# Optimization experiments

Hardware: AMD Instinct MI355X
Metric: run time of the kernel (lower is better)

## Reference

```python
import jax, jax.numpy as jnp
import numpy as np

D_MODEL = 1024
N_HEADS = 16
D_KV = 64
N_CONTEXT = 20
PASSAGE_LEN = 200
BSZ = 8
QLEN = 32
KLEN = N_CONTEXT * PASSAGE_LEN


def setup_inputs() -> dict:
    key = jax.random.key(0)
    ks = jax.random.split(key, 8)
    inp = {
        "input": jax.random.normal(ks[0], (BSZ, QLEN, D_MODEL), jnp.float32),
        "kv": jax.random.normal(ks[1], (BSZ, KLEN, D_MODEL), jnp.float32),
        "mask_add": jnp.zeros((BSZ, 1, 1, KLEN), jnp.float32),
        "mask_bool": jnp.ones((BSZ, 1, 1, KLEN), bool),
        "position_bias": jax.random.normal(ks[2], (1, N_HEADS, QLEN, KLEN), jnp.float32),
        "Wq": jax.random.normal(ks[3], (D_MODEL, N_HEADS * D_KV), jnp.float32) * 0.02,
        "Wk": jax.random.normal(ks[4], (D_MODEL, N_HEADS * D_KV), jnp.float32) * 0.02,
        "Wv": jax.random.normal(ks[5], (D_MODEL, N_HEADS * D_KV), jnp.float32) * 0.02,
        "Wo": jax.random.normal(ks[6], (N_HEADS * D_KV, D_MODEL), jnp.float32) * 0.02,
        "n_context": N_CONTEXT,
    }
    return inp


def reference(input, kv, mask_add, mask_bool, position_bias, Wq, Wk, Wv, Wo, n_context):
    b, qlen, dm = input.shape
    klen = kv.shape[1]
    H = position_bias.shape[1]
    dh = Wq.shape[1] // H
    # projections, [b, h, len, dh]
    q = (input @ Wq).reshape(b, qlen, H, dh).transpose(0, 2, 1, 3)
    k = (kv @ Wk).reshape(b, klen, H, dh).transpose(0, 2, 1, 3)
    v = (kv @ Wv).reshape(b, klen, H, dh).transpose(0, 2, 1, 3)
    # unscaled T5-style attention scores + additive mask + position bias
    scores = jnp.einsum('bhqd,bhkd->bhqk', q, k) + mask_add + position_bias
    attn = jax.nn.softmax(scores.astype(jnp.float32), axis=-1).astype(scores.dtype)
    # dropout p=0 (eval) -> identity
    out = jnp.einsum('bhqk,bhkd->bhqd', attn, v)
    out = out.transpose(0, 2, 1, 3).reshape(b, qlen, H * dh) @ Wo
    # collect_cross_attention(sum_over_tokens=True): masked avg of raw scores per context
    s = scores.reshape(b, H, qlen, n_context, -1)
    m = mask_bool.reshape(b, 1, 1, n_context, -1).astype(scores.dtype)
    collected = (s * m).sum(-1) / m.sum(-1)  # [b, H, qlen, n_context]
    return out, collected
```

## Files before the change

### kernel.cpp

```cpp
#include <hip/hip_runtime.h>
#include <stdint.h>

constexpr int DMODEL = 1024;
constexpr int NH     = 16;
constexpr int DHD    = 64;
constexpr int BS     = 8;
constexpr int QLEN   = 32;
constexpr int KLEN   = 4000;
constexpr int NCTX   = 20;
constexpr int PLEN   = 200;

typedef __bf16 bf16_t;
typedef bf16_t bf16x8 __attribute__((ext_vector_type(8)));
typedef float  f32x4  __attribute__((ext_vector_type(4)));

__device__ __forceinline__ uint16_t f2bf(float f) {
  uint32_t u = __float_as_uint(f);
  u += 0x7FFF + ((u >> 16) & 1);
  return (uint16_t)(u >> 16);
}

#define GLOAD_LDS16(gsrc, ldst) \
  __builtin_amdgcn_global_load_lds((const __attribute__((address_space(1))) void*)(gsrc), \
                                   (__attribute__((address_space(3))) void*)(ldst), 16, 0, 0)

__global__ void detect_mask(const uint32_t* __restrict__ m, int* __restrict__ flag) {
  if (threadIdx.x == 0 && blockIdx.x == 0)
    *flag = (m[0] == 0x01010101u) ? 1 : 0;
}

__global__ void cast_inputs(const float* __restrict__ kv, const float* __restrict__ inp,
                            uint16_t* __restrict__ kv16, uint16_t* __restrict__ in16) {
  const int NKV4 = (BS * KLEN * DMODEL) / 4;
  const int NIN4 = (BS * QLEN * DMODEL) / 4;
  const int total = NKV4 + NIN4;
  for (int i = blockIdx.x * blockDim.x + threadIdx.x; i < total; i += gridDim.x * blockDim.x) {
    float4 v; uint16_t* dst; int di;
    if (i < NKV4) { v = ((const float4*)kv)[i]; dst = kv16; di = i; }
    else          { v = ((const float4*)inp)[i - NKV4]; dst = in16; di = i - NKV4; }
    ushort4 o; o.x = f2bf(v.x); o.y = f2bf(v.y); o.z = f2bf(v.z); o.w = f2bf(v.w);
    ((ushort4*)dst)[di] = o;
  }
}

__global__ void wtrans(const float* __restrict__ w0, const float* __restrict__ w1,
                       const float* __restrict__ w2, const float* __restrict__ w3,
                       uint16_t* __restrict__ out) {
  __shared__ uint16_t sm[64][65];
  const float* W = (blockIdx.z == 0) ? w0 : (blockIdx.z == 1) ? w1 : (blockIdx.z == 2) ? w2 : w3;
  uint16_t* o = out + (size_t)blockIdx.z * DMODEL * DMODEL;
  int k0 = blockIdx.y * 64, n0 = blockIdx.x * 64;
  int t = threadIdx.x;
  for (int i = 0; i < 16; ++i) {
    int s = t + i * 256; int r = s >> 6, c = s & 63;
    sm[r][c] = f2bf(W[(size_t)(k0 + r) * DMODEL + n0 + c]);
  }
  __syncthreads();
  for (int i = 0; i < 16; ++i) {
    int s = t + i * 256; int r = s >> 6, c = s & 63;
    o[(size_t)(n0 + r) * DMODEL + k0 + c] = sm[c][r];
  }
}

template <int OUT_F32>
__global__ void __launch_bounds__(256) gemm_bt(const uint16_t* __restrict__ A,
                                               const uint16_t* __restrict__ Bt,
                                               void* __restrict__ Cv,
                                               int M, int N, int K) {
  __shared__ __align__(16) uint16_t As[128 * 32];
  __shared__ __align__(16) uint16_t Bs[128 * 32];
  const int m0 = blockIdx.x * 128, n0 = blockIdx.y * 128;
  const int tid = threadIdx.x, lane = tid & 63, wave = tid >> 6;
  const int wm = wave >> 1, wn = wave & 1;
  const int l15 = lane & 15, g = lane >> 4;
  const int sr = lane >> 2, sc = (lane & 3) * 8;
  const int c0 = wave * 2, c1 = wave * 2 + 1;
  f32x4 acc[4][4] = {};
  const int KT = K / 32;
  for (int kt = 0; kt < KT; ++kt) {
    __syncthreads();
    GLOAD_LDS16(A  + (size_t)(m0 + c0 * 16 + sr) * K + kt * 32 + sc, As + c0 * 512);
    GLOAD_LDS16(A  + (size_t)(m0 + c1 * 16 + sr) * K + kt * 32 + sc, As + c1 * 512);
    GLOAD_LDS16(Bt + (size_t)(n0 + c0 * 16 + sr) * K + kt * 32 + sc, Bs + c0 * 512);
    GLOAD_LDS16(Bt + (size_t)(n0 + c1 * 16 + sr) * K + kt * 32 + sc, Bs + c1 * 512);
    __syncthreads();
    bf16x8 a[4], b[4];
#pragma unroll
    for (int i = 0; i < 4; ++i)
      a[i] = *(const bf16x8*)&As[(wm * 64 + i * 16 + l15) * 32 + g * 8];
#pragma unroll
    for (int j = 0; j < 4; ++j)
      b[j] = *(const bf16x8*)&Bs[(wn * 64 + j * 16 + l15) * 32 + g * 8];
#pragma unroll
    for (int i = 0; i < 4; ++i)
#pragma unroll
      for (int j = 0; j < 4; ++j)
        acc[i][j] = __builtin_amdgcn_mfma_f32_16x16x32_bf16(a[i], b[j], acc[i][j], 0, 0, 0);
  }
#pragma unroll
  for (int i = 0; i < 4; ++i)
#pragma unroll
    for (int j = 0; j < 4; ++j) {
      int row = m0 + wm * 64 + i * 16 + g * 4;
      int col = n0 + wn * 64 + j * 16 + l15;
      if (OUT_F32) {
        float* C = (float*)Cv;
#pragma unroll
        for (int r = 0; r < 4; ++r) C[(size_t)(row + r) * N + col] = acc[i][j][r];
      } else {
        uint16_t* C = (uint16_t*)Cv;
#pragma unroll
        for (int r = 0; r < 4; ++r) C[(size_t)(row + r) * N + col] = f2bf(acc[i][j][r]);
      }
    }
}

__global__ void __launch_bounds__(512) gemm_kv(const uint16_t* __restrict__ A,
                                               const uint16_t* __restrict__ Bt,
                                               uint16_t* __restrict__ kmat,
                                               uint16_t* __restrict__ vt) {
  __shared__ __align__(16) uint16_t smem[65536];
  const int orig = blockIdx.x;
  const int swz  = (orig & 7) * 125 + (orig >> 3);
  const int mb = swz >> 3, nb = swz & 7;
  const int m0 = mb * 256, n0 = nb * 256;
  const int tid = threadIdx.x, lane = tid & 63, wid = tid >> 6;
  const int wm = wid >> 2, wn = wid & 3;
  const int l15 = lane & 15, g = lane >> 4;
  const int l3 = lane >> 3, l7 = lane & 7;
  const int cg = (l7 ^ (l3 & 7)) * 8;

  f32x4 acc[8][4] = {};

#define ABASE(bf) (smem + (bf) * 32768)
#define BBASE(bf) (smem + (bf) * 32768 + 16384)

  auto STAGE = [&](int bf, int kt) {
    const int colg = kt * 64 + cg;
#pragma unroll
    for (int ia = 0; ia < 4; ++ia) {
      const int r0 = wid * 32 + ia * 8;
      GLOAD_LDS16(A + (size_t)(m0 + r0 + l3) * 1024 + colg, ABASE(bf) + r0 * 64);
    }
#pragma unroll
    for (int ib = 0; ib < 4; ++ib) {
      const int r0 = wid * 32 + ib * 8;
      GLOAD_LDS16(Bt + (size_t)(n0 + r0 + l3) * 1024 + colg, BBASE(bf) + r0 * 64);
    }
  };

  STAGE(0, 0);
  for (int kt = 0; kt < 16; ++kt) {
    const int bf = kt & 1;
    if (kt < 15) {
      STAGE(bf ^ 1, kt + 1);
      asm volatile("s_waitcnt vmcnt(8)" ::: "memory");
    } else {
      asm volatile("s_waitcnt vmcnt(0)" ::: "memory");
    }
    asm volatile("s_barrier" ::: "memory");
#pragma unroll
    for (int kk = 0; kk < 2; ++kk) {
      bf16x8 af[8], bb[4];
#pragma unroll
      for (int mi = 0; mi < 8; ++mi) {
        const int row = wm * 128 + mi * 16 + l15;
        const int gr = (kk * 4 + g) ^ (row & 7);
        af[mi] = *(const bf16x8*)&ABASE(bf)[row * 64 + gr * 8];
      }
#pragma unroll
      for (int ni = 0; ni < 4; ++ni) {
        const int row = wn * 64 + ni * 16 + l15;
        const int gr = (kk * 4 + g) ^ (row & 7);
        bb[ni] = *(const bf16x8*)&BBASE(bf)[row * 64 + gr * 8];
      }
#pragma unroll
      for (int mi = 0; mi < 8; ++mi)
#pragma unroll
        for (int ni = 0; ni < 4; ++ni)
          acc[mi][ni] = __builtin_amdgcn_mfma_f32_16x16x32_bf16(af[mi], bb[ni], acc[mi][ni], 0, 0, 0);
    }
    asm volatile("s_barrier" ::: "memory");
  }
#undef ABASE
#undef BBASE

  if (n0 < 1024) {
#pragma unroll
    for (int mi = 0; mi < 8; ++mi)
#pragma unroll
      for (int ni = 0; ni < 4; ++ni) {
        const int row = m0 + wm * 128 + mi * 16 + g * 4;
        const int col = n0 + wn * 64 + ni * 16 + l15;
#pragma unroll
        for (int r = 0; r < 4; ++r)
          kmat[(size_t)(row + r) * 1024 + col] = f2bf(acc[mi][ni][r]);
      }
  } else {
#pragma unroll
    for (int mi = 0; mi < 8; ++mi)
#pragma unroll
      for (int ni = 0; ni < 4; ++ni) {
        const int dd = wn * 64 + ni * 16 + l15;
        const int kk_tok = wm * 128 + mi * 16 + g * 4;
#pragma unroll
        for (int r = 0; r < 4; ++r)
          smem[dd * 256 + kk_tok + r] = f2bf(acc[mi][ni][r]);
      }
    __syncthreads();
    const int hbase = (n0 - 1024) >> 6;
#pragma unroll
    for (int it = 0; it < 16; ++it) {
      const int sp = it * 512 + tid;
      const int dd = sp >> 5, kk0 = (sp & 31) * 8;
      const int grow = m0 + kk0;
      const int b = grow / 4000, krel = grow - b * 4000;
      const int h = hbase + (dd >> 6), d = dd & 63;
      ulonglong2 v = *(const ulonglong2*)&smem[dd * 256 + kk0];
      *(ulonglong2*)&vt[(((size_t)(b * NH + h) * DHD + d) * KLEN) + krel] = v;
    }
  }
}

__global__ void __launch_bounds__(256) fused_attn(const uint16_t* __restrict__ Q,
                                                  const uint16_t* __restrict__ Km,
                                                  const uint16_t* __restrict__ Vt,
                                                  const float* __restrict__ mask_add,
                                                  const void* __restrict__ maskb,
                                                  const int* __restrict__ flag,
                                                  const float* __restrict__ bias,
                                                  float* __restrict__ part,
                                                  float* __restrict__ coll) {
  __shared__ __align__(16) uint16_t plds[4][32 * 32];
  const int kc = blockIdx.x, h = blockIdx.y, b = blockIdx.z;
  const int lane = threadIdx.x & 63, wave = threadIdx.x >> 6;
  const int l15 = lane & 15, g = lane >> 4;
  const int ctx = kc * 4 + wave;
  const int kbase = ctx * PLEN;
  const int fm = *flag;

  bf16x8 aq[2][2];
#pragma unroll
  for (int i = 0; i < 2; ++i)
#pragma unroll
    for (int ks = 0; ks < 2; ++ks)
      aq[i][ks] = *(const bf16x8*)&Q[(size_t)(b * QLEN + i * 16 + l15) * DMODEL + h * DHD + ks * 32 + g * 8];

  f32x4 o[2][4] = {};
  float mr[2][4], lr[2][4], cs[2][4];
#pragma unroll
  for (int i = 0; i < 2; ++i)
#pragma unroll
    for (int r = 0; r < 4; ++r) { mr[i][r] = -3e38f; lr[i][r] = 0.f; cs[i][r] = 0.f; }
  float cnt = 0.f;

  for (int t = 0; t < 7; ++t) {
    const int k0 = kbase + t * 32;
    bf16x8 kb[2][2];
#pragma unroll
    for (int j = 0; j < 2; ++j) {
      int kr = k0 + j * 16 + l15; if (kr > KLEN - 1) kr = KLEN - 1;
#pragma unroll
      for (int ks = 0; ks < 2; ++ks)
        kb[j][ks] = *(const bf16x8*)&Km[(size_t)(b * KLEN + kr) * DMODEL + h * DHD + ks * 32 + g * 8];
    }
    f32x4 sa[2][2] = {};
#pragma unroll
    for (int ks = 0; ks < 2; ++ks)
#pragma unroll
      for (int i = 0; i < 2; ++i)
#pragma unroll
        for (int j = 0; j < 2; ++j)
          sa[i][j] = __builtin_amdgcn_mfma_f32_16x16x32_bf16(aq[i][ks], kb[j][ks], sa[i][j], 0, 0, 0);

    int colc[2]; bool vd[2], vm[2]; float ma[2];
#pragma unroll
    for (int j = 0; j < 2; ++j) {
      int col = k0 + j * 16 + l15;
      vd[j] = (col < kbase + PLEN);
      int cc = col; if (cc > KLEN - 1) cc = KLEN - 1;
      colc[j] = cc;
      ma[j] = mask_add[b * KLEN + cc];
      bool mk = fm ? (((const uint8_t*)maskb)[b * KLEN + cc] != 0)
                   : (((const int*)maskb)[b * KLEN + cc] != 0);
      vm[j] = vd[j] && mk;
    }

    float sv[2][2][4];
    float tmax[2][4];
#pragma unroll
    for (int i = 0; i < 2; ++i)
#pragma unroll
      for (int r = 0; r < 4; ++r) {
        tmax[i][r] = -3e38f;
        const int q = i * 16 + g * 4 + r;
        const size_t brow = (size_t)(h * QLEN + q) * KLEN;
#pragma unroll
        for (int j = 0; j < 2; ++j) {
          float raw = sa[i][j][r] + ma[j] + bias[brow + colc[j]];
          cs[i][r] += vm[j] ? raw : 0.f;
          float x = vd[j] ? raw : -3e38f;
          sv[i][j][r] = x;
          tmax[i][r] = fmaxf(tmax[i][r], x);
        }
      }
#pragma unroll
    for (int j = 0; j < 2; ++j) cnt += vm[j] ? 1.f : 0.f;

#pragma unroll
    for (int i = 0; i < 2; ++i)
#pragma unroll
      for (int r = 0; r < 4; ++r) {
        float v = tmax[i][r];
        v = fmaxf(v, __shfl_xor(v, 1)); v = fmaxf(v, __shfl_xor(v, 2));
        v = fmaxf(v, __shfl_xor(v, 4)); v = fmaxf(v, __shfl_xor(v, 8));
        tmax[i][r] = v;
      }
    float scale[2][4];
#pragma unroll
    for (int i = 0; i < 2; ++i)
#pragma unroll
      for (int r = 0; r < 4; ++r) {
        float mn = fmaxf(mr[i][r], tmax[i][r]);
        scale[i][r] = __expf(mr[i][r] - mn);
        mr[i][r] = mn;
        lr[i][r] *= scale[i][r];
      }
#pragma unroll
    for (int i = 0; i < 2; ++i)
#pragma unroll
      for (int j2 = 0; j2 < 4; ++j2)
#pragma unroll
        for (int r = 0; r < 4; ++r)
          o[i][j2][r] *= scale[i][r];
#pragma unroll
    for (int i = 0; i < 2; ++i)
#pragma unroll
      for (int r = 0; r < 4; ++r) {
        const int q = i * 16 + g * 4 + r;
#pragma unroll
        for (int j = 0; j < 2; ++j) {
          float p = __expf(sv[i][j][r] - mr[i][r]);
          lr[i][r] += p;
          plds[wave][q * 32 + j * 16 + l15] = f2bf(p);
        }
      }
    bf16x8 ap[2];
#pragma unroll
    for (int i = 0; i < 2; ++i)
      ap[i] = *(const bf16x8*)&plds[wave][(i * 16 + l15) * 32 + g * 8];
    bf16x8 vb[4];
    int vc = k0 + g * 8; if (vc > KLEN - 8) vc = KLEN - 8;
#pragma unroll
    for (int j2 = 0; j2 < 4; ++j2)
      vb[j2] = *(const bf16x8*)&Vt[((size_t)((b * NH + h) * DHD + j2 * 16 + l15)) * KLEN + vc];
#pragma unroll
    for (int i = 0; i < 2; ++i)
#pragma unroll
      for (int j2 = 0; j2 < 4; ++j2)
        o[i][j2] = __builtin_amdgcn_mfma_f32_16x16x32_bf16(ap[i], vb[j2], o[i][j2], 0, 0, 0);
  }

#pragma unroll
  for (int i = 0; i < 2; ++i)
#pragma unroll
    for (int r = 0; r < 4; ++r) {
      float v = lr[i][r];
      v += __shfl_xor(v, 1); v += __shfl_xor(v, 2); v += __shfl_xor(v, 4); v += __shfl_xor(v, 8);
      lr[i][r] = v;
      float c = cs[i][r];
      c += __shfl_xor(c, 1); c += __shfl_xor(c, 2); c += __shfl_xor(c, 4); c += __shfl_xor(c, 8);
      cs[i][r] = c;
    }
  { float c = cnt; c += __shfl_xor(c, 1); c += __shfl_xor(c, 2); c += __shfl_xor(c, 4); c += __shfl_xor(c, 8); cnt = c; }

  float* pr = part + ((size_t)((b * NH + h) * NCTX + ctx)) * 32 * 72;
#pragma unroll
  for (int i = 0; i < 2; ++i)
#pragma unroll
    for (int j2 = 0; j2 < 4; ++j2)
#pragma unroll
      for (int r = 0; r < 4; ++r)
        pr[(i * 16 + g * 4 + r) * 72 + 8 + j2 * 16 + l15] = o[i][j2][r];
  if (l15 == 0) {
#pragma unroll
    for (int i = 0; i < 2; ++i)
#pragma unroll
      for (int r = 0; r < 4; ++r) {
        int q = i * 16 + g * 4 + r;
        pr[q * 72 + 0] = mr[i][r];
        pr[q * 72 + 1] = lr[i][r];
        coll[(((size_t)(b * NH + h)) * QLEN + q) * NCTX + ctx] = cs[i][r] / cnt;
      }
  }
}

__global__ void __launch_bounds__(256) combine_attn(const float* __restrict__ part,
                                                    uint16_t* __restrict__ ao16) {
  const int t = threadIdx.x;
  const int row = blockIdx.x * 16 + (t >> 4);
  const int ln = t & 15;
  const int bh = row >> 5, q = row & 31;
  const float* p0 = part + ((size_t)bh * 640 + q) * 72;
  float M = -3e38f;
#pragma unroll
  for (int c = 0; c < NCTX; ++c) M = fmaxf(M, p0[(size_t)c * 2304]);
  float Z = 0.f, o0 = 0.f, o1 = 0.f, o2 = 0.f, o3 = 0.f;
  const int d0 = ln * 4;
  for (int c = 0; c < NCTX; ++c) {
    const float* pc = p0 + (size_t)c * 2304;
    float e = __expf(pc[0] - M);
    Z += e * pc[1];
    float4 ov = *(const float4*)&pc[8 + d0];
    o0 += e * ov.x; o1 += e * ov.y; o2 += e * ov.z; o3 += e * ov.w;
  }
  float iz = 1.f / Z;
  const int b = bh >> 4, h = bh & 15;
  ushort4 w; w.x = f2bf(o0 * iz); w.y = f2bf(o1 * iz); w.z = f2bf(o2 * iz); w.w = f2bf(o3 * iz);
  *(ushort4*)&ao16[(size_t)(b * QLEN + q) * DMODEL + h * DHD + d0] = w;
}

extern "C" void kernel_launch(void* const* d_in, const int* in_sizes, int n_in,
                              void* d_out, int out_size, void* d_ws, size_t ws_size,
                              hipStream_t stream) {
  const float* input     = (const float*)d_in[0];
  const float* kv        = (const float*)d_in[1];
  const float* mask_add  = (const float*)d_in[2];
  const void*  mask_bool = d_in[3];
  const float* bias      = (const float*)d_in[4];
  const float* Wq        = (const float*)d_in[5];
  const float* Wk        = (const float*)d_in[6];
  const float* Wv        = (const float*)d_in[7];
  const float* Wo        = (const float*)d_in[8];
  float* out  = (float*)d_out;
  float* coll = out + (size_t)BS * QLEN * DMODEL;

  char* ws = (char*)d_ws;
  size_t off = 0;
  auto alloc = [&](size_t bytes) { char* p = ws + off; off += (bytes + 255) & ~(size_t)255; return p; };
  uint16_t* kv16 = (uint16_t*)alloc((size_t)BS * KLEN * DMODEL * 2);
  uint16_t* in16 = (uint16_t*)alloc((size_t)BS * QLEN * DMODEL * 2);
  uint16_t* wt   = (uint16_t*)alloc((size_t)4 * DMODEL * DMODEL * 2);
  uint16_t* q16  = (uint16_t*)alloc((size_t)BS * QLEN * DMODEL * 2);
  uint16_t* kmat = (uint16_t*)alloc((size_t)BS * KLEN * DMODEL * 2);
  uint16_t* vt   = (uint16_t*)alloc((size_t)BS * KLEN * DMODEL * 2);
  float*    part = (float*)   alloc((size_t)BS * NH * NCTX * 32 * 72 * 4);
  uint16_t* ao16 = (uint16_t*)alloc((size_t)BS * QLEN * DMODEL * 2);
  int*      flag = (int*)alloc(256);

  uint16_t* WqT  = wt;
  uint16_t* WkvT = wt + (size_t)DMODEL * DMODEL;
  uint16_t* WoT  = wt + (size_t)3 * DMODEL * DMODEL;

  detect_mask<<<1, 64, 0, stream>>>((const uint32_t*)mask_bool, flag);
  cast_inputs<<<2048, 256, 0, stream>>>(kv, input, kv16, in16);
  wtrans<<<dim3(16, 16, 4), 256, 0, stream>>>(Wq, Wk, Wv, Wo, wt);
  gemm_bt<0><<<dim3(2, 8), 256, 0, stream>>>(in16, WqT, q16, BS * QLEN, DMODEL, DMODEL);
  gemm_kv<<<1000, 512, 0, stream>>>(kv16, WkvT, kmat, vt);
  fused_attn<<<dim3(5, NH, BS), 256, 0, stream>>>(q16, kmat, vt, mask_add, mask_bool, flag,
                                                  bias, part, coll);
  combine_attn<<<256, 256, 0, stream>>>(part, ao16);
  gemm_bt<1><<<dim3(2, 8), 256, 0, stream>>>(ao16, WoT, out, BS * QLEN, DMODEL, DMODEL);
}
```

Baseline: 305.3 us.

## Fuse fp32-to-bf16 cast of kv into the K/V projection GEMM loader

Removes the separate cast pass over the large kv tensor. The K/V GEMM now reads fp32 kv directly, converts it to bf16 with packed conversion instructions, and writes it into swizzled LDS. This avoids writing and re-reading a bf16 copy of kv. In exchange, the A-operand load is no longer an async global-to-LDS prefetch: it is a synchronous register load in the same iteration, so it loses the overlap with compute and doubles A read bytes per tile. Each kv row is also re-read and re-converted by every N-block.

```diff
diff --git a/kernel.cpp b/kernel.cpp
--- a/kernel.cpp
+++ b/kernel.cpp
@@ -29,18 +29,11 @@
     *flag = (m[0] == 0x01010101u) ? 1 : 0;
 }
 
-__global__ void cast_inputs(const float* __restrict__ kv, const float* __restrict__ inp,
-                            uint16_t* __restrict__ kv16, uint16_t* __restrict__ in16) {
-  const int NKV4 = (BS * KLEN * DMODEL) / 4;
-  const int NIN4 = (BS * QLEN * DMODEL) / 4;
-  const int total = NKV4 + NIN4;
-  for (int i = blockIdx.x * blockDim.x + threadIdx.x; i < total; i += gridDim.x * blockDim.x) {
-    float4 v; uint16_t* dst; int di;
-    if (i < NKV4) { v = ((const float4*)kv)[i]; dst = kv16; di = i; }
-    else          { v = ((const float4*)inp)[i - NKV4]; dst = in16; di = i - NKV4; }
-    ushort4 o; o.x = f2bf(v.x); o.y = f2bf(v.y); o.z = f2bf(v.z); o.w = f2bf(v.w);
-    ((ushort4*)dst)[di] = o;
-  }
+__global__ void cast_in16(const float* __restrict__ inp, uint16_t* __restrict__ in16) {
+  int i = blockIdx.x * blockDim.x + threadIdx.x;
+  float4 v = ((const float4*)inp)[i];
+  ushort4 o; o.x = f2bf(v.x); o.y = f2bf(v.y); o.z = f2bf(v.z); o.w = f2bf(v.w);
+  ((ushort4*)in16)[i] = o;
 }
 
 __global__ void wtrans(const float* __restrict__ w0, const float* __restrict__ w1,
@@ -115,7 +108,7 @@
     }
 }
 
-__global__ void __launch_bounds__(512) gemm_kv(const uint16_t* __restrict__ A,
+__global__ void __launch_bounds__(512) gemm_kv(const float* __restrict__ A,
                                                const uint16_t* __restrict__ Bt,
                                                uint16_t* __restrict__ kmat,
                                                uint16_t* __restrict__ vt) {
@@ -130,33 +123,47 @@
   const int l3 = lane >> 3, l7 = lane & 7;
   const int cg = (l7 ^ (l3 & 7)) * 8;
 
+  int ar0 = tid >> 3;
   f32x4 acc[8][4] = {};
 
 #define ABASE(bf) (smem + (bf) * 32768)
 #define BBASE(bf) (smem + (bf) * 32768 + 16384)
 
-  auto STAGE = [&](int bf, int kt) {
-    const int colg = kt * 64 + cg;
-#pragma unroll
-    for (int ia = 0; ia < 4; ++ia) {
-      const int r0 = wid * 32 + ia * 8;
-      GLOAD_LDS16(A + (size_t)(m0 + r0 + l3) * 1024 + colg, ABASE(bf) + r0 * 64);
-    }
+  auto STAGE_B = [&](int bf, int kt) {
 #pragma unroll
     for (int ib = 0; ib < 4; ++ib) {
       const int r0 = wid * 32 + ib * 8;
-      GLOAD_LDS16(Bt + (size_t)(n0 + r0 + l3) * 1024 + colg, BBASE(bf) + r0 * 64);
+      GLOAD_LDS16(Bt + (size_t)(n0 + r0 + l3) * 1024 + kt * 64 + cg, BBASE(bf) + r0 * 64);
     }
   };
 
-  STAGE(0, 0);
+  STAGE_B(0, 0);
   for (int kt = 0; kt < 16; ++kt) {
     const int bf = kt & 1;
+    float4 a8[8];
+#pragma unroll
+    for (int p = 0; p < 4; ++p) {
+      const int s = p * 512 + tid, r = s >> 3, gw = s & 7;
+      const float* src = A + (size_t)(m0 + r) * 1024 + kt * 64 + gw * 8;
+      a8[2 * p]     = *(const float4*)(src);
+      a8[2 * p + 1] = *(const float4*)(src + 4);
+    }
+#pragma unroll
+    for (int p = 0; p < 4; ++p) {
+      const int s = p * 512 + tid, r = s >> 3, gw = s & 7;
+      uint32_t w0, w1, w2, w3;
+      asm("v_cvt_pk_bf16_f32 %0, %1, %2" : "=v"(w0) : "v"(a8[2 * p].x),     "v"(a8[2 * p].y));
+      asm("v_cvt_pk_bf16_f32 %0, %1, %2" : "=v"(w1) : "v"(a8[2 * p].z),     "v"(a8[2 * p].w));
+      asm("v_cvt_pk_bf16_f32 %0, %1, %2" : "=v"(w2) : "v"(a8[2 * p + 1].x), "v"(a8[2 * p + 1].y));
+      asm("v_cvt_pk_bf16_f32 %0, %1, %2" : "=v"(w3) : "v"(a8[2 * p + 1].z), "v"(a8[2 * p + 1].w));
+      uint4 wv; wv.x = w0; wv.y = w1; wv.z = w2; wv.w = w3;
+      *(uint4*)&ABASE(bf)[r * 64 + (gw ^ (r & 7)) * 8] = wv;
+    }
     if (kt < 15) {
-      STAGE(bf ^ 1, kt + 1);
-      asm volatile("s_waitcnt vmcnt(8)" ::: "memory");
+      STAGE_B(bf ^ 1, kt + 1);
+      asm volatile("s_waitcnt vmcnt(4) lgkmcnt(0)" ::: "memory");
     } else {
-      asm volatile("s_waitcnt vmcnt(0)" ::: "memory");
+      asm volatile("s_waitcnt vmcnt(0) lgkmcnt(0)" ::: "memory");
     }
     asm volatile("s_barrier" ::: "memory");
 #pragma unroll
@@ -438,7 +445,6 @@
   char* ws = (char*)d_ws;
   size_t off = 0;
   auto alloc = [&](size_t bytes) { char* p = ws + off; off += (bytes + 255) & ~(size_t)255; return p; };
-  uint16_t* kv16 = (uint16_t*)alloc((size_t)BS * KLEN * DMODEL * 2);
   uint16_t* in16 = (uint16_t*)alloc((size_t)BS * QLEN * DMODEL * 2);
   uint16_t* wt   = (uint16_t*)alloc((size_t)4 * DMODEL * DMODEL * 2);
   uint16_t* q16  = (uint16_t*)alloc((size_t)BS * QLEN * DMODEL * 2);
@@ -453,10 +459,10 @@
   uint16_t* WoT  = wt + (size_t)3 * DMODEL * DMODEL;
 
   detect_mask<<<1, 64, 0, stream>>>((const uint32_t*)mask_bool, flag);
-  cast_inputs<<<2048, 256, 0, stream>>>(kv, input, kv16, in16);
+  cast_in16<<<256, 256, 0, stream>>>(input, in16);
   wtrans<<<dim3(16, 16, 4), 256, 0, stream>>>(Wq, Wk, Wv, Wo, wt);
   gemm_bt<0><<<dim3(2, 8), 256, 0, stream>>>(in16, WqT, q16, BS * QLEN, DMODEL, DMODEL);
-  gemm_kv<<<1000, 512, 0, stream>>>(kv16, WkvT, kmat, vt);
+  gemm_kv<<<1000, 512, 0, stream>>>(kv, WkvT, kmat, vt);
   fused_attn<<<dim3(5, NH, BS), 256, 0, stream>>>(q16, kmat, vt, mask_add, mask_bool, flag,
                                                   bias, part, coll);
   combine_attn<<<256, 256, 0, stream>>>(part, ao16);
```

Measured after the change: 349.9 us. 1.15x slower.
